# Kernel optimization log

Hardware: AMD Instinct MI355X
Metric: run time of the kernel (lower is better)

The kernel has to match this reference:

```python
import jax, jax.numpy as jnp
import numpy as np

HEAD_DIM = 6
WS = 8  # window size
GROUPS = 4
EPS = 1e-5


def conv3x3(x, w, b):
    y = jax.lax.conv_general_dilated(x, w, (1, 1), [(1, 1), (1, 1)],
                                     dimension_numbers=('NCHW', 'OIHW', 'NCHW'))
    return y + b[None, :, None, None]


def conv1x1(x, w, b):
    # w: (O, C, 1, 1) pointwise conv == channel matmul
    return jnp.einsum('bchw,oc->bohw', x, w[:, :, 0, 0]) + b[None, :, None, None]


def group_norm(x, gamma, beta):
    B, C, H, W = x.shape
    xg = x.reshape(B, GROUPS, C // GROUPS, H, W)
    mu = xg.mean(axis=(2, 3, 4), keepdims=True)
    var = xg.var(axis=(2, 3, 4), keepdims=True)
    xg = (xg - mu) * jax.lax.rsqrt(var + EPS)
    return xg.reshape(B, C, H, W) * gamma[None, :, None, None] + beta[None, :, None, None]


def window_attention(x, qkv_w, qkv_b, proj_w, proj_b):
    # Per-window channel attention (attn is head_dim x head_dim, softmax over last dim).
    B, C, H, W = x.shape
    heads = C // HEAD_DIM
    scale = HEAD_DIM ** -0.5
    Hn, Wn = H // WS, W // WS
    L = WS * WS
    qkv = conv1x1(x, qkv_w, qkv_b)                       # (B, 3C, H, W); 1x1 conv commutes with windowing
    qkv = qkv.reshape(B, 3, heads, HEAD_DIM, Hn, WS, Wn, WS)
    qkv = qkv.transpose(1, 0, 4, 6, 2, 3, 5, 7).reshape(3, B, Hn, Wn, heads, HEAD_DIM, L)
    q, k, v = qkv[0], qkv[1], qkv[2]
    attn = jnp.einsum('bijhdl,bijhel->bijhde', q, k) * scale  # (B,Hn,Wn,heads,hd,hd)
    attn = jax.nn.softmax(attn, axis=-1)
    out = jnp.einsum('bijhde,bijhel->bijhdl', attn, v)
    out = out.reshape(B, Hn, Wn, heads, HEAD_DIM, WS, WS)
    out = out.transpose(0, 3, 4, 1, 5, 2, 6).reshape(B, C, H, W)
    return conv1x1(out, proj_w, proj_b)


def shifted_window_attention(x, qkv_w, qkv_b, proj_w, proj_b):
    B, C, H, W = x.shape
    pad_h = (WS - H % WS) % WS
    pad_w = (WS - W % WS) % WS
    if pad_h or pad_w:
        x = jnp.pad(x, ((0, 0), (0, 0), (0, pad_h), (0, pad_w)), mode='reflect')
    s = WS // 2
    x_sh = jnp.roll(x, shift=(-s, -s), axis=(2, 3))
    x1 = window_attention(x, qkv_w, qkv_b, proj_w, proj_b)
    x2 = window_attention(x_sh, qkv_w, qkv_b, proj_w, proj_b)
    x2 = jnp.roll(x2, shift=(s, s), axis=(2, 3))
    x = (x1 + x2) * 0.5
    return x[:, :, :H, :W]


def setup_inputs() -> dict:
    key = jax.random.key(0)
    ks = jax.random.split(key, 12)
    B, Cin, Cout, T, H, W = 16, 96, 96, 256, 128, 128
    std = 0.05
    return {
        'x': jax.random.normal(ks[0], (B, Cin, H, W), jnp.float32),
        't_emb': jax.random.normal(ks[1], (B, T), jnp.float32),
        'w1': jax.random.normal(ks[2], (Cout, Cin, 3, 3), jnp.float32) * std,
        'b1': jnp.zeros((Cout,), jnp.float32),
        'g1': jnp.ones((Cout,), jnp.float32),
        'be1': jnp.zeros((Cout,), jnp.float32),
        'wt': jax.random.normal(ks[3], (2 * Cout, T), jnp.float32) * std,
        'bt': jnp.zeros((2 * Cout,), jnp.float32),
        'qkv_w': jax.random.normal(ks[4], (3 * Cout, Cout, 1, 1), jnp.float32) * std,
        'qkv_b': jnp.zeros((3 * Cout,), jnp.float32),
        'proj_w': jax.random.normal(ks[5], (Cout, Cout, 1, 1), jnp.float32) * std,
        'proj_b': jnp.zeros((Cout,), jnp.float32),
        'ga': jnp.ones((Cout,), jnp.float32),
        'ba': jnp.zeros((Cout,), jnp.float32),
        'w2': jax.random.normal(ks[6], (Cout, Cout, 3, 3), jnp.float32) * std,
        'b2': jnp.zeros((Cout,), jnp.float32),
        'g2': jnp.ones((Cout,), jnp.float32),
        'be2': jnp.zeros((Cout,), jnp.float32),
    }


def reference(x, t_emb, w1, b1, g1, be1, wt, bt, qkv_w, qkv_b, proj_w, proj_b,
              ga, ba, w2, b2, g2, be2):
    C = w1.shape[0]
    # layer1: conv3x3 -> GN(4) -> SiLU
    h = jax.nn.silu(group_norm(conv3x3(x, w1, b1), g1, be1))
    # time FiLM
    t = jax.nn.silu(t_emb @ wt.T + bt)             # (B, 2C)
    shift, bias = t[:, :C], t[:, C:]
    h = h * (1.0 + shift[:, :, None, None]) + bias[:, :, None, None]
    residual = h
    h = group_norm(h, ga, ba)
    h = shifted_window_attention(h, qkv_w, qkv_b, proj_w, proj_b)
    h = residual + h
    # layer2: conv3x3 -> GN(4) -> SiLU
    h = jax.nn.silu(group_norm(conv3x3(h, w2, b2), g2, be2))
    return h
```

## Files before the change

### kernel.cpp

```cpp
#include <hip/hip_runtime.h>

#define B_   16
#define C_   96
#define H_   128
#define W_   128
#define HW_  16384
#define CPG_ 24
#define NPG_ 393216.0f
#define TDIM_ 256
#define PLANE_ ((size_t)B_ * C_ * HW_)

typedef unsigned short ushort_t;
typedef __bf16 bf16x8 __attribute__((ext_vector_type(8)));
typedef float  f32x4  __attribute__((ext_vector_type(4)));
typedef unsigned short u16x8 __attribute__((ext_vector_type(8)));
typedef unsigned short u16x4 __attribute__((ext_vector_type(4)));

#define ICP 104

__device__ __forceinline__ float silu_f(float x) { return x / (1.f + __expf(-x)); }
__device__ __forceinline__ float bf2f(ushort_t u) {
    union { float f; unsigned int i; } x; x.i = ((unsigned int)u) << 16; return x.f;
}
__device__ __forceinline__ ushort_t f2bf(float f) {
    __bf16 h = (__bf16)f; return *(ushort_t*)&h;
}

__global__ void temb_kernel(const float* __restrict__ t_emb,
                            const float* __restrict__ wt,
                            const float* __restrict__ bt,
                            float* __restrict__ tvec) {
    int idx = blockIdx.x * 256 + threadIdx.x;
    if (idx >= B_ * 192) return;
    int b = idx / 192, o = idx - b * 192;
    float a = bt[o];
    const float* te = t_emb + b * TDIM_;
    const float* wr = wt + o * TDIM_;
    for (int k = 0; k < TDIM_; ++k) a += te[k] * wr[k];
    tvec[idx] = silu_f(a);
}

__global__ void castw_kernel(const float* __restrict__ w1,
                             const float* __restrict__ w2,
                             ushort_t* __restrict__ wbf1,
                             ushort_t* __restrict__ wbf2) {
    int i = blockIdx.x * 256 + threadIdx.x;
    int ic = i % 96;
    int t  = i / 96;
    int oc = t % 96;
    int kk = t / 96;
    int src = (oc * 96 + ic) * 9 + kk;
    wbf1[i] = f2bf(w1[src]);
    wbf2[i] = f2bf(w2[src]);
}

template<int FP32>
__device__ __forceinline__ void stage_row(const void* __restrict__ xin,
                                          ushort_t* __restrict__ ti2,
                                          int b, int gy, int x0, int slot, int tid) {
    const bool rowok = (gy >= 0 && gy < H_);
#pragma unroll
    for (int it = 0; it < 3; ++it) {
        int idx = it * 256 + tid;
        int ic = idx % 96;
        int xc = idx / 96;
        u16x8 v = {};
        if (rowok) {
            if (FP32) {
                const float* xf = (const float*)xin;
                const float4* p = (const float4*)&xf[((size_t)(b * 96 + ic) * H_ + gy) * W_ + x0 + xc * 8];
                float4 f0 = p[0], f1 = p[1];
                v[0] = f2bf(f0.x); v[1] = f2bf(f0.y); v[2] = f2bf(f0.z); v[3] = f2bf(f0.w);
                v[4] = f2bf(f1.x); v[5] = f2bf(f1.y); v[6] = f2bf(f1.z); v[7] = f2bf(f1.w);
            } else {
                const ushort_t* xb = (const ushort_t*)xin;
                v = *(const u16x8*)&xb[((size_t)(b * 96 + ic) * H_ + gy) * W_ + x0 + xc * 8];
            }
        }
        ushort_t* dst = &ti2[(slot * 66 + xc * 8 + 1) * ICP + ic];
#pragma unroll
        for (int j = 0; j < 8; ++j) dst[j * ICP] = v[j];
    }
    if (tid < 192) {
        int ic = tid % 96;
        int side = tid / 96;
        int xi = side ? 65 : 0;
        int gx = x0 - 1 + xi;
        ushort_t vv = 0;
        if (rowok && gx >= 0 && gx < W_) {
            if (FP32) vv = f2bf(((const float*)xin)[((size_t)(b * 96 + ic) * H_ + gy) * W_ + gx]);
            else      vv = ((const ushort_t*)xin)[((size_t)(b * 96 + ic) * H_ + gy) * W_ + gx];
        }
        ti2[(slot * 66 + xi) * ICP + ic] = vv;
    }
}

template<int FP32>
__global__ __launch_bounds__(256, 3)
void conv3x3_mfma_kernel(const void* __restrict__ xin,
                         const ushort_t* __restrict__ wbf,
                         const float* __restrict__ bias,
                         float* __restrict__ out,
                         float* __restrict__ stats) {
    __shared__ __align__(16) ushort_t ti2[2 * 66 * ICP];
    __shared__ __align__(16) ushort_t wc[96 * ICP];
    __shared__ float red[4][96][2];

    const int b   = blockIdx.z;
    const int y0  = blockIdx.y * 2;
    const int x0  = blockIdx.x * 64;
    const int tid = threadIdx.x;
    const int wv   = tid >> 6;
    const int lane = tid & 63;
    const int l15  = lane & 15;
    const int quad = lane >> 4;

    stage_row<FP32>(xin, ti2, b, y0 - 1, x0, 0, tid);
    stage_row<FP32>(xin, ti2, b, y0 + 0, x0, 1, tid);

    int wsrc[5], wdst[5];
#pragma unroll
    for (int i = 0; i < 5; ++i) {
        int idx = tid + i * 256;
        int icb = idx % 12;
        int oc  = idx / 12;
        wsrc[i] = oc * 96 + icb * 8;
        wdst[i] = oc * ICP + icb * 8;
    }
    u16x8 wreg[5];
#pragma unroll
    for (int i = 0; i < 4; ++i) wreg[i] = *(const u16x8*)&wbf[wsrc[i]];
    if (tid < 128) wreg[4] = *(const u16x8*)&wbf[wsrc[4]];

    f32x4 acc[2][6];
#pragma unroll
    for (int m = 0; m < 2; ++m)
#pragma unroll
        for (int nt = 0; nt < 6; ++nt)
            acc[m][nt] = (f32x4){0.f, 0.f, 0.f, 0.f};

#pragma unroll 1
    for (int kk = 0; kk < 9; ++kk) {
        const int ky = (kk >= 6) ? 2 : (kk >= 3 ? 1 : 0);
        const int kx = kk - 3 * ky;
        const int sA = ky & 1;
        const int sB = sA ^ 1;

        __syncthreads();
#pragma unroll
        for (int i = 0; i < 4; ++i) *(u16x8*)&wc[wdst[i]] = wreg[i];
        if (tid < 128) *(u16x8*)&wc[wdst[4]] = wreg[4];
        if (kk == 3)      stage_row<FP32>(xin, ti2, b, y0 + 1, x0, 0, tid);
        else if (kk == 6) stage_row<FP32>(xin, ti2, b, y0 + 2, x0, 1, tid);
        __syncthreads();
        if (kk < 8) {
            const ushort_t* wsk = wbf + (kk + 1) * 9216;
#pragma unroll
            for (int i = 0; i < 4; ++i) wreg[i] = *(const u16x8*)&wsk[wsrc[i]];
            if (tid < 128) wreg[4] = *(const u16x8*)&wsk[wsrc[4]];
        }
#pragma unroll 1
        for (int ck = 0; ck < 3; ++ck) {
            const int kbase = ck * 32 + quad * 8;
            bf16x8 a0 = *(const bf16x8*)&ti2[(sA * 66 + (wv * 16 + l15 + kx)) * ICP + kbase];
            bf16x8 a1 = *(const bf16x8*)&ti2[(sB * 66 + (wv * 16 + l15 + kx)) * ICP + kbase];
#pragma unroll
            for (int nt = 0; nt < 6; ++nt) {
                bf16x8 bv = *(const bf16x8*)&wc[(nt * 16 + l15) * ICP + kbase];
                acc[0][nt] = __builtin_amdgcn_mfma_f32_16x16x32_bf16(a0, bv, acc[0][nt], 0, 0, 0);
                acc[1][nt] = __builtin_amdgcn_mfma_f32_16x16x32_bf16(a1, bv, acc[1][nt], 0, 0, 0);
            }
        }
    }

    float lsum[6], lsq[6];
#pragma unroll
    for (int nt = 0; nt < 6; ++nt) { lsum[nt] = 0.f; lsq[nt] = 0.f; }

#pragma unroll
    for (int m = 0; m < 2; ++m) {
        const int gy = y0 + m;
        const int gx = x0 + wv * 16 + quad * 4;
#pragma unroll
        for (int nt = 0; nt < 6; ++nt) {
            const int oc = nt * 16 + l15;
            const float bz = bias[oc];
            float v0 = acc[m][nt][0] + bz;
            float v1 = acc[m][nt][1] + bz;
            float v2 = acc[m][nt][2] + bz;
            float v3 = acc[m][nt][3] + bz;
            float4 vv = make_float4(v0, v1, v2, v3);
            *(float4*)&out[((size_t)(b * 96 + oc) * H_ + gy) * W_ + gx] = vv;
            lsum[nt] += v0 + v1 + v2 + v3;
            lsq[nt]  += v0 * v0 + v1 * v1 + v2 * v2 + v3 * v3;
        }
    }
#pragma unroll
    for (int nt = 0; nt < 6; ++nt) {
        float s = lsum[nt], q = lsq[nt];
        s += __shfl_down(s, 32, 64);
        s += __shfl_down(s, 16, 64);
        q += __shfl_down(q, 32, 64);
        q += __shfl_down(q, 16, 64);
        if (lane < 16) {
            red[wv][nt * 16 + lane][0] = s;
            red[wv][nt * 16 + lane][1] = q;
        }
    }
    __syncthreads();
    if (tid < 8) {
        const int g = tid >> 1, which = tid & 1;
        float v = 0.f;
        for (int oc = g * CPG_; oc < g * CPG_ + CPG_; ++oc)
            for (int w2 = 0; w2 < 4; ++w2) v += red[w2][oc][which];
        atomicAdd(&stats[(b * 4 + g) * 2 + which], v);
    }
}

__global__ void apply1_kernel(const float* y,
                              const float* __restrict__ stats1,
                              const float* __restrict__ g1,
                              const float* __restrict__ be1,
                              const float* __restrict__ tvec,
                              float* h,
                              float* __restrict__ stats2) {
    const int bc = blockIdx.x;
    const int b = bc / C_, c = bc - b * C_;
    const int g = c / CPG_;
    const float sum = stats1[(b * 4 + g) * 2], sumsq = stats1[(b * 4 + g) * 2 + 1];
    const float mean = sum / NPG_;
    const float var  = sumsq / NPG_ - mean * mean;
    const float rstd = rsqrtf(var + 1e-5f);
    const float sc = rstd * g1[c];
    const float sh = be1[c] - mean * sc;
    const float tsc = 1.f + tvec[b * 192 + c];
    const float tbi = tvec[b * 192 + 96 + c];

    const float4* yp = (const float4*)(y + (size_t)bc * HW_);
    float4* hp = (float4*)(h + (size_t)bc * HW_);
    float ls = 0.f, lss = 0.f;
    for (int i = threadIdx.x; i < HW_ / 4; i += 256) {
        float4 v = yp[i];
        float r0 = silu_f(v.x * sc + sh) * tsc + tbi;
        float r1 = silu_f(v.y * sc + sh) * tsc + tbi;
        float r2 = silu_f(v.z * sc + sh) * tsc + tbi;
        float r3 = silu_f(v.w * sc + sh) * tsc + tbi;
        hp[i] = make_float4(r0, r1, r2, r3);
        ls  += r0 + r1 + r2 + r3;
        lss += r0*r0 + r1*r1 + r2*r2 + r3*r3;
    }
    for (int off = 32; off > 0; off >>= 1) {
        ls  += __shfl_down(ls, off, 64);
        lss += __shfl_down(lss, off, 64);
    }
    if ((threadIdx.x & 63) == 0) {
        atomicAdd(&stats2[(b * 4 + g) * 2 + 0], ls);
        atomicAdd(&stats2[(b * 4 + g) * 2 + 1], lss);
    }
}

__global__ void gn_bf16_kernel(const float* __restrict__ in,
                               const float* __restrict__ stats,
                               const float* __restrict__ gamma,
                               const float* __restrict__ beta,
                               ushort_t* __restrict__ outb) {
    const int bc = blockIdx.x;
    const int b = bc / C_, c = bc - b * C_;
    const int g = c / CPG_;
    const float sum = stats[(b * 4 + g) * 2], sumsq = stats[(b * 4 + g) * 2 + 1];
    const float mean = sum / NPG_;
    const float var  = sumsq / NPG_ - mean * mean;
    const float rstd = rsqrtf(var + 1e-5f);
    const float sc = rstd * gamma[c];
    const float sh = beta[c] - mean * sc;
    const float4* ip = (const float4*)(in + (size_t)bc * HW_);
    ushort4* op = (ushort4*)(outb + (size_t)bc * HW_);
    for (int i = threadIdx.x; i < HW_ / 4; i += 256) {
        float4 v = ip[i];
        ushort4 u = { f2bf(v.x * sc + sh), f2bf(v.y * sc + sh),
                      f2bf(v.z * sc + sh), f2bf(v.w * sc + sh) };
        op[i] = u;
    }
}

__global__ void gn_apply_kernel(const float* in,
                                const float* __restrict__ stats,
                                const float* __restrict__ gamma,
                                const float* __restrict__ beta,
                                float* out, int dosilu) {
    const int bc = blockIdx.x;
    const int b = bc / C_, c = bc - b * C_;
    const int g = c / CPG_;
    const float sum = stats[(b * 4 + g) * 2], sumsq = stats[(b * 4 + g) * 2 + 1];
    const float mean = sum / NPG_;
    const float var  = sumsq / NPG_ - mean * mean;
    const float rstd = rsqrtf(var + 1e-5f);
    const float sc = rstd * gamma[c];
    const float sh = beta[c] - mean * sc;
    const float4* ip = (const float4*)(in + (size_t)bc * HW_);
    float4* op = (float4*)(out + (size_t)bc * HW_);
    for (int i = threadIdx.x; i < HW_ / 4; i += 256) {
        float4 v = ip[i];
        float r0 = v.x * sc + sh, r1 = v.y * sc + sh;
        float r2 = v.z * sc + sh, r3 = v.w * sc + sh;
        if (dosilu) { r0 = silu_f(r0); r1 = silu_f(r1); r2 = silu_f(r2); r3 = silu_f(r3); }
        op[i] = make_float4(r0, r1, r2, r3);
    }
}

__global__ __launch_bounds__(256, 3)
void qkv_gemm_kernel(const ushort_t* __restrict__ xq,
                     const float* __restrict__ qw,
                     const float* __restrict__ qb,
                     ushort_t* __restrict__ qkvbuf) {
    __shared__ __align__(16) ushort_t ti[2 * 64 * ICP];
    __shared__ __align__(16) ushort_t wc[96 * ICP];

    const int bz = blockIdx.z;
    const int b = bz / 3, s = bz - b * 3;
    const int y0 = blockIdx.y * 2;
    const int x0 = blockIdx.x * 64;
    const int tid = threadIdx.x;
    const int wv = tid >> 6, lane = tid & 63;
    const int l15 = lane & 15, quad = lane >> 4;

#pragma unroll
    for (int it = 0; it < 6; ++it) {
        int idx = it * 256 + tid;
        int ic = idx % 96;
        int t2 = idx / 96;
        int xc = t2 & 7;
        int r  = t2 >> 3;
        u16x8 v = *(const u16x8*)&xq[((size_t)(b * 96 + ic) * H_ + y0 + r) * W_ + x0 + xc * 8];
        ushort_t* dst = &ti[(r * 64 + xc * 8) * ICP + ic];
#pragma unroll
        for (int j = 0; j < 8; ++j) dst[j * ICP] = v[j];
    }
#pragma unroll
    for (int it = 0; it < 9; ++it) {
        int idx = it * 256 + tid;
        int icq = idx % 24;
        int oc  = idx / 24;
        float4 wv4 = *(const float4*)&qw[(s * 96 + oc) * 96 + icq * 4];
        ushort4 u = { f2bf(wv4.x), f2bf(wv4.y), f2bf(wv4.z), f2bf(wv4.w) };
        *(ushort4*)&wc[oc * ICP + icq * 4] = u;
    }
    __syncthreads();

    f32x4 acc[2][6];
#pragma unroll
    for (int m = 0; m < 2; ++m)
#pragma unroll
        for (int nt = 0; nt < 6; ++nt) acc[m][nt] = (f32x4){0.f, 0.f, 0.f, 0.f};

#pragma unroll
    for (int ck = 0; ck < 3; ++ck) {
        const int kbase = ck * 32 + quad * 8;
        bf16x8 a0 = *(const bf16x8*)&ti[(0 * 64 + wv * 16 + l15) * ICP + kbase];
        bf16x8 a1 = *(const bf16x8*)&ti[(1 * 64 + wv * 16 + l15) * ICP + kbase];
#pragma unroll
        for (int nt = 0; nt < 6; ++nt) {
            bf16x8 bv = *(const bf16x8*)&wc[(nt * 16 + l15) * ICP + kbase];
            acc[0][nt] = __builtin_amdgcn_mfma_f32_16x16x32_bf16(a0, bv, acc[0][nt], 0, 0, 0);
            acc[1][nt] = __builtin_amdgcn_mfma_f32_16x16x32_bf16(a1, bv, acc[1][nt], 0, 0, 0);
        }
    }

#pragma unroll
    for (int m = 0; m < 2; ++m) {
        const int gy = y0 + m;
        const int gx = x0 + wv * 16 + quad * 4;
#pragma unroll
        for (int nt = 0; nt < 6; ++nt) {
            const int ocg = s * 96 + nt * 16 + l15;
            const float bz2 = qb[ocg];
            ushort4 u = { f2bf(acc[m][nt][0] + bz2), f2bf(acc[m][nt][1] + bz2),
                          f2bf(acc[m][nt][2] + bz2), f2bf(acc[m][nt][3] + bz2) };
            *(ushort4*)&qkvbuf[((size_t)(b * 288 + ocg) * H_ + gy) * W_ + gx] = u;
        }
    }
}

#define QKC 1288
#define QKR 160
#define OSTS 1032
#define VTS 520
__global__ __launch_bounds__(256, 2)
void attn2_kernel(const ushort_t* __restrict__ qkv,
                  ushort_t* __restrict__ obuf, int shift, int accumulate) {
    __shared__ __align__(16) ushort_t qk[12 * QKC];
    __shared__ __align__(16) ushort_t vt[16 * VTS + 32];
    __shared__ __align__(16) ushort_t ost[6 * OSTS];

    const int h = blockIdx.x, wy = blockIdx.y, b = blockIdx.z;
    const int tid = threadIdx.x;
    const int wv = tid >> 6, lane = tid & 63;
    const int l15 = lane & 15, quad = lane >> 4;

    for (int idx = tid; idx < 2304; idx += 256) {
        int xc = idx & 15;
        int t2 = idx >> 4;
        int r  = t2 & 7;
        int ch = t2 >> 3;
        int part = ch / 6, d = ch - part * 6;
        int gch = part * 96 + h * 6 + d;
        int gy = (wy * 8 + r + shift) & 127;
        size_t rowb = ((size_t)(b * 288 + gch) * H_ + gy) * W_;
        ushort4 u0, u1;
        if (shift == 0) {
            u0 = *(const ushort4*)&qkv[rowb + xc * 8];
            u1 = *(const ushort4*)&qkv[rowb + xc * 8 + 4];
        } else {
            u0 = *(const ushort4*)&qkv[rowb + ((xc * 8 + 4) & 127)];
            u1 = *(const ushort4*)&qkv[rowb + ((xc * 8 + 8) & 127)];
        }
        ushort_t* dst = (part < 2) ? &qk[ch * QKC + r * QKR + xc * 8]
                                   : &ost[d * OSTS + r * 128 + xc * 8];
        *(ushort4*)dst = u0;
        *(ushort4*)(dst + 4) = u1;
    }
    __syncthreads();

    {
        const int r   = tid >> 5;
        const int pxq = tid & 31;
        const int px  = pxq * 4;
        u16x4 vv[6];
#pragma unroll
        for (int c = 0; c < 6; ++c)
            vv[c] = *(const u16x4*)&ost[c * OSTS + r * 128 + px];
        const int wx = px >> 3;
        const int p7 = px & 7;
#pragma unroll
        for (int j = 0; j < 4; ++j) {
            u16x8 t;
            t[0] = vv[0][j]; t[1] = vv[1][j]; t[2] = vv[2][j];
            t[3] = vv[3][j]; t[4] = vv[4][j]; t[5] = vv[5][j];
            t[6] = 0; t[7] = 0;
            *(u16x8*)&vt[wx * VTS + (r * 8 + p7 + j) * 8] = t;
        }
        if (tid < 16) ((unsigned int*)(vt + 16 * VTS))[tid] = 0u;
    }
    __syncthreads();

    const float scale = 0.40824829046386302f;
    const int dcl = (l15 < 6) ? l15 : 5;
    const int chA = 6 + dcl;
    const int chB = dcl;

    for (int i = 0; i < 4; ++i) {
        const int wx = wv * 4 + i;
        f32x4 sa = (f32x4){0.f, 0.f, 0.f, 0.f};
#pragma unroll
        for (int ck = 0; ck < 2; ++ck) {
            const int r = ck * 4 + quad;
            bf16x8 af  = *(const bf16x8*)&qk[chA * QKC + r * QKR + wx * 8];
            bf16x8 bfv = *(const bf16x8*)&qk[chB * QKC + r * QKR + wx * 8];
            sa = __builtin_amdgcn_mfma_f32_16x16x32_bf16(af, bfv, sa, 0, 0, 0);
        }
        float s0 = sa[0] * scale, s1 = sa[1] * scale, s2 = sa[2] * scale, s3 = sa[3] * scale;
        float m = -3.4e38f;
        if (quad == 0) m = fmaxf(fmaxf(s0, s1), fmaxf(s2, s3));
        else if (quad == 1) m = fmaxf(s0, s1);
        m = fmaxf(m, __shfl_xor(m, 16, 64));
        m = fmaxf(m, __shfl_xor(m, 32, 64));
        float p0 = (quad <= 1) ? __expf(s0 - m) : 0.f;
        float p1 = (quad <= 1) ? __expf(s1 - m) : 0.f;
        float p2 = (quad == 0) ? __expf(s2 - m) : 0.f;
        float p3 = (quad == 0) ? __expf(s3 - m) : 0.f;
        float sum = p0 + p1 + p2 + p3;
        sum += __shfl_xor(sum, 16, 64);
        sum += __shfl_xor(sum, 32, 64);
        float inv = 1.f / sum;
        p0 *= inv; p1 *= inv; p2 *= inv; p3 *= inv;
        float e4 = __shfl_xor(p0, 16, 64);
        float e5 = __shfl_xor(p1, 16, 64);
        bf16x8 pf;
        pf[0] = (__bf16)p0; pf[1] = (__bf16)p1; pf[2] = (__bf16)p2; pf[3] = (__bf16)p3;
        pf[4] = (__bf16)e4; pf[5] = (__bf16)e5;
        pf[6] = (__bf16)0.f; pf[7] = (__bf16)0.f;
        if (quad != 0) { bf16x8 z = {}; pf = z; }
#pragma unroll
        for (int mt = 0; mt < 4; ++mt) {
            bf16x8 av = *(const bf16x8*)&vt[wx * VTS + (mt * 16 + l15) * 8 + quad * 8];
            f32x4 o = __builtin_amdgcn_mfma_f32_16x16x32_bf16(av, pf, (f32x4){0.f,0.f,0.f,0.f}, 0, 0, 0);
            if (l15 < 6) {
                const int px = mt * 16 + quad * 4;
                const int r = px >> 3, c = px & 7;
                ushort4 st = { f2bf(o[0]), f2bf(o[1]), f2bf(o[2]), f2bf(o[3]) };
                *(ushort4*)&ost[l15 * OSTS + r * 128 + wx * 8 + c] = st;
            }
        }
    }
    __syncthreads();

    for (int idx = tid; idx < 768; idx += 256) {
        int xc = idx & 15;
        int t2 = idx >> 4;
        int r = t2 & 7, d = t2 >> 3;
        int gy = (wy * 8 + r + shift) & 127;
        size_t rowb = ((size_t)(b * 96 + h * 6 + d) * H_ + gy) * W_;
        size_t a0, a1;
        if (shift == 0) { a0 = rowb + xc * 8; a1 = rowb + xc * 8 + 4; }
        else { a0 = rowb + ((xc * 8 + 4) & 127); a1 = rowb + ((xc * 8 + 8) & 127); }
        const ushort_t* src = &ost[d * OSTS + r * 128 + xc * 8];
        ushort4 v0 = *(const ushort4*)src;
        ushort4 v1 = *(const ushort4*)(src + 4);
        if (accumulate) {
            ushort4 q0 = *(const ushort4*)&obuf[a0];
            ushort4 q1 = *(const ushort4*)&obuf[a1];
            v0.x = f2bf(0.5f * (bf2f(v0.x) + bf2f(q0.x)));
            v0.y = f2bf(0.5f * (bf2f(v0.y) + bf2f(q0.y)));
            v0.z = f2bf(0.5f * (bf2f(v0.z) + bf2f(q0.z)));
            v0.w = f2bf(0.5f * (bf2f(v0.w) + bf2f(q0.w)));
            v1.x = f2bf(0.5f * (bf2f(v1.x) + bf2f(q1.x)));
            v1.y = f2bf(0.5f * (bf2f(v1.y) + bf2f(q1.y)));
            v1.z = f2bf(0.5f * (bf2f(v1.z) + bf2f(q1.z)));
            v1.w = f2bf(0.5f * (bf2f(v1.w) + bf2f(q1.w)));
        }
        *(ushort4*)&obuf[a0] = v0;
        *(ushort4*)&obuf[a1] = v1;
    }
}

__global__ __launch_bounds__(256, 3)
void proj_gemm_kernel(const ushort_t* __restrict__ ob,
                      const float* __restrict__ pw,
                      const float* __restrict__ pb,
                      const float* __restrict__ resid,
                      ushort_t* __restrict__ h2) {
    __shared__ __align__(16) ushort_t ti[2 * 64 * ICP];
    __shared__ __align__(16) ushort_t wc[96 * ICP];

    const int b = blockIdx.z;
    const int y0 = blockIdx.y * 2;
    const int x0 = blockIdx.x * 64;
    const int tid = threadIdx.x;
    const int wv = tid >> 6, lane = tid & 63;
    const int l15 = lane & 15, quad = lane >> 4;

#pragma unroll
    for (int it = 0; it < 6; ++it) {
        int idx = it * 256 + tid;
        int ic = idx % 96;
        int t2 = idx / 96;
        int xc = t2 & 7;
        int r  = t2 >> 3;
        u16x8 v = *(const u16x8*)&ob[((size_t)(b * 96 + ic) * H_ + y0 + r) * W_ + x0 + xc * 8];
        ushort_t* dst = &ti[(r * 64 + xc * 8) * ICP + ic];
#pragma unroll
        for (int j = 0; j < 8; ++j) dst[j * ICP] = v[j];
    }
#pragma unroll
    for (int it = 0; it < 9; ++it) {
        int idx = it * 256 + tid;
        int icq = idx % 24;
        int oc  = idx / 24;
        float4 wv4 = *(const float4*)&pw[oc * 96 + icq * 4];
        ushort4 u = { f2bf(wv4.x), f2bf(wv4.y), f2bf(wv4.z), f2bf(wv4.w) };
        *(ushort4*)&wc[oc * ICP + icq * 4] = u;
    }
    __syncthreads();

    f32x4 acc[2][6];
#pragma unroll
    for (int m = 0; m < 2; ++m)
#pragma unroll
        for (int nt = 0; nt < 6; ++nt) acc[m][nt] = (f32x4){0.f, 0.f, 0.f, 0.f};

#pragma unroll
    for (int ck = 0; ck < 3; ++ck) {
        const int kbase = ck * 32 + quad * 8;
        bf16x8 a0 = *(const bf16x8*)&ti[(0 * 64 + wv * 16 + l15) * ICP + kbase];
        bf16x8 a1 = *(const bf16x8*)&ti[(1 * 64 + wv * 16 + l15) * ICP + kbase];
#pragma unroll
        for (int nt = 0; nt < 6; ++nt) {
            bf16x8 bv = *(const bf16x8*)&wc[(nt * 16 + l15) * ICP + kbase];
            acc[0][nt] = __builtin_amdgcn_mfma_f32_16x16x32_bf16(a0, bv, acc[0][nt], 0, 0, 0);
            acc[1][nt] = __builtin_amdgcn_mfma_f32_16x16x32_bf16(a1, bv, acc[1][nt], 0, 0, 0);
        }
    }

#pragma unroll
    for (int m = 0; m < 2; ++m) {
        const int gy = y0 + m;
        const int gx = x0 + wv * 16 + quad * 4;
#pragma unroll
        for (int nt = 0; nt < 6; ++nt) {
            const int oc = nt * 16 + l15;
            const float bz2 = pb[oc];
            size_t addr = ((size_t)(b * 96 + oc) * H_ + gy) * W_ + gx;
            float4 rv = *(const float4*)&resid[addr];
            ushort4 u = { f2bf(acc[m][nt][0] + bz2 + rv.x),
                          f2bf(acc[m][nt][1] + bz2 + rv.y),
                          f2bf(acc[m][nt][2] + bz2 + rv.z),
                          f2bf(acc[m][nt][3] + bz2 + rv.w) };
            *(ushort4*)&h2[addr] = u;
        }
    }
}

extern "C" void kernel_launch(void* const* d_in, const int* in_sizes, int n_in,
                              void* d_out, int out_size, void* d_ws, size_t ws_size,
                              hipStream_t stream) {
    const float* x     = (const float*)d_in[0];
    const float* t_emb = (const float*)d_in[1];
    const float* w1    = (const float*)d_in[2];
    const float* b1    = (const float*)d_in[3];
    const float* g1    = (const float*)d_in[4];
    const float* be1   = (const float*)d_in[5];
    const float* wt    = (const float*)d_in[6];
    const float* bt    = (const float*)d_in[7];
    const float* qkv_w = (const float*)d_in[8];
    const float* qkv_b = (const float*)d_in[9];
    const float* proj_w= (const float*)d_in[10];
    const float* proj_b= (const float*)d_in[11];
    const float* ga    = (const float*)d_in[12];
    const float* ba    = (const float*)d_in[13];
    const float* w2    = (const float*)d_in[14];
    const float* b2    = (const float*)d_in[15];
    const float* g2    = (const float*)d_in[16];
    const float* be2   = (const float*)d_in[17];

    float* out = (float*)d_out;

    ushort_t* A  = (ushort_t*)d_ws;
    ushort_t* Bq = A + PLANE_;
    float* stats = (float*)(Bq + 3 * PLANE_);
    float* tvec  = stats + 384;
    ushort_t* wbf1 = (ushort_t*)(tvec + 3072);
    ushort_t* wbf2 = wbf1 + 82944;

    hipMemsetAsync(stats, 0, 384 * sizeof(float), stream);
    temb_kernel<<<12, 256, 0, stream>>>(t_emb, wt, bt, tvec);
    castw_kernel<<<324, 256, 0, stream>>>(w1, w2, wbf1, wbf2);

    conv3x3_mfma_kernel<1><<<dim3(2, 64, 16), 256, 0, stream>>>((const void*)x, wbf1, b1, out, stats);

    apply1_kernel<<<B_ * C_, 256, 0, stream>>>(out, stats, g1, be1, tvec, out, stats + 128);
    gn_bf16_kernel<<<B_ * C_, 256, 0, stream>>>(out, stats + 128, ga, ba, A);

    qkv_gemm_kernel<<<dim3(2, 64, 48), 256, 0, stream>>>(A, qkv_w, qkv_b, Bq);

    attn2_kernel<<<dim3(16, 16, 16), 256, 0, stream>>>(Bq, A, 0, 0);
    attn2_kernel<<<dim3(16, 16, 16), 256, 0, stream>>>(Bq, A, 4, 1);

    proj_gemm_kernel<<<dim3(2, 64, 16), 256, 0, stream>>>(A, proj_w, proj_b, out, Bq);

    conv3x3_mfma_kernel<0><<<dim3(2, 64, 16), 256, 0, stream>>>((const void*)Bq, wbf2, b2, out, stats + 256);

    gn_apply_kernel<<<B_ * C_, 256, 0, stream>>>(out, stats + 256, g2, be2, out, 1);
}
```

Before: 727.1 us.

## Load conv3x3 weights straight into registers in MFMA layout with 4-row tiles

Weights are now pre-permuted on the host-side cast kernel into the per-lane MFMA fragment order, so each lane reads its B fragments directly from global memory into registers with double-buffered prefetch. This removes the shared-memory weight staging and the two barriers per filter tap. Each block now computes four output rows instead of two, using a 4-slot rolling row buffer, which halves the grid and reuses each weight fragment across more MFMAs. The cost is more accumulator registers (occupancy hint lowered to 2 blocks) and weight reads that go to global or L2 per block rather than shared memory.

```diff
diff --git a/kernel.cpp b/kernel.cpp
--- a/kernel.cpp
+++ b/kernel.cpp
@@ -45,10 +45,14 @@
                              ushort_t* __restrict__ wbf1,
                              ushort_t* __restrict__ wbf2) {
     int i = blockIdx.x * 256 + threadIdx.x;
-    int ic = i % 96;
-    int t  = i / 96;
-    int oc = t % 96;
-    int kk = t / 96;
+    int j    = i & 7;
+    int lane = (i >> 3) & 63;
+    int t    = i >> 9;
+    int nt   = t % 6;
+    int ks   = t / 6;
+    int kk   = ks / 3, ck = ks - 3 * kk;
+    int oc = nt * 16 + (lane & 15);
+    int ic = ck * 32 + (lane >> 4) * 8 + j;
     int src = (oc * 96 + ic) * 9 + kk;
     wbf1[i] = f2bf(w1[src]);
     wbf2[i] = f2bf(w2[src]);
@@ -96,18 +100,17 @@
 }
 
 template<int FP32>
-__global__ __launch_bounds__(256, 3)
+__global__ __launch_bounds__(256, 2)
 void conv3x3_mfma_kernel(const void* __restrict__ xin,
                          const ushort_t* __restrict__ wbf,
                          const float* __restrict__ bias,
                          float* __restrict__ out,
                          float* __restrict__ stats) {
-    __shared__ __align__(16) ushort_t ti2[2 * 66 * ICP];
-    __shared__ __align__(16) ushort_t wc[96 * ICP];
+    __shared__ __align__(16) ushort_t ti2[4 * 66 * ICP];
     __shared__ float red[4][96][2];
 
     const int b   = blockIdx.z;
-    const int y0  = blockIdx.y * 2;
+    const int y0  = blockIdx.y * 4;
     const int x0  = blockIdx.x * 64;
     const int tid = threadIdx.x;
     const int wv   = tid >> 6;
@@ -117,60 +120,61 @@
 
     stage_row<FP32>(xin, ti2, b, y0 - 1, x0, 0, tid);
     stage_row<FP32>(xin, ti2, b, y0 + 0, x0, 1, tid);
-
-    int wsrc[5], wdst[5];
-#pragma unroll
-    for (int i = 0; i < 5; ++i) {
-        int idx = tid + i * 256;
-        int icb = idx % 12;
-        int oc  = idx / 12;
-        wsrc[i] = oc * 96 + icb * 8;
-        wdst[i] = oc * ICP + icb * 8;
-    }
-    u16x8 wreg[5];
-#pragma unroll
-    for (int i = 0; i < 4; ++i) wreg[i] = *(const u16x8*)&wbf[wsrc[i]];
-    if (tid < 128) wreg[4] = *(const u16x8*)&wbf[wsrc[4]];
-
-    f32x4 acc[2][6];
-#pragma unroll
-    for (int m = 0; m < 2; ++m)
+    stage_row<FP32>(xin, ti2, b, y0 + 1, x0, 2, tid);
+    stage_row<FP32>(xin, ti2, b, y0 + 2, x0, 3, tid);
+
+    const ushort_t* wrp = wbf + (size_t)lane * 8;
+
+    bf16x8 wA[6], wB[6];
+#pragma unroll
+    for (int nt = 0; nt < 6; ++nt)
+        wA[nt] = *(const bf16x8*)&wrp[nt * 512];
+
+    f32x4 acc[4][6];
+#pragma unroll
+    for (int m = 0; m < 4; ++m)
 #pragma unroll
         for (int nt = 0; nt < 6; ++nt)
             acc[m][nt] = (f32x4){0.f, 0.f, 0.f, 0.f};
 
-#pragma unroll 1
-    for (int kk = 0; kk < 9; ++kk) {
-        const int ky = (kk >= 6) ? 2 : (kk >= 3 ? 1 : 0);
-        const int kx = kk - 3 * ky;
-        const int sA = ky & 1;
-        const int sB = sA ^ 1;
-
-        __syncthreads();
-#pragma unroll
-        for (int i = 0; i < 4; ++i) *(u16x8*)&wc[wdst[i]] = wreg[i];
-        if (tid < 128) *(u16x8*)&wc[wdst[4]] = wreg[4];
-        if (kk == 3)      stage_row<FP32>(xin, ti2, b, y0 + 1, x0, 0, tid);
-        else if (kk == 6) stage_row<FP32>(xin, ti2, b, y0 + 2, x0, 1, tid);
-        __syncthreads();
-        if (kk < 8) {
-            const ushort_t* wsk = wbf + (kk + 1) * 9216;
-#pragma unroll
-            for (int i = 0; i < 4; ++i) wreg[i] = *(const u16x8*)&wsk[wsrc[i]];
-            if (tid < 128) wreg[4] = *(const u16x8*)&wsk[wsrc[4]];
-        }
-#pragma unroll 1
-        for (int ck = 0; ck < 3; ++ck) {
-            const int kbase = ck * 32 + quad * 8;
-            bf16x8 a0 = *(const bf16x8*)&ti2[(sA * 66 + (wv * 16 + l15 + kx)) * ICP + kbase];
-            bf16x8 a1 = *(const bf16x8*)&ti2[(sB * 66 + (wv * 16 + l15 + kx)) * ICP + kbase];
-#pragma unroll
-            for (int nt = 0; nt < 6; ++nt) {
-                bf16x8 bv = *(const bf16x8*)&wc[(nt * 16 + l15) * ICP + kbase];
-                acc[0][nt] = __builtin_amdgcn_mfma_f32_16x16x32_bf16(a0, bv, acc[0][nt], 0, 0, 0);
-                acc[1][nt] = __builtin_amdgcn_mfma_f32_16x16x32_bf16(a1, bv, acc[1][nt], 0, 0, 0);
-            }
-        }
+    __syncthreads();
+
+    auto body = [&](int ks, bf16x8 (&cur)[6], bf16x8 (&nxt)[6]) {
+        const int kk = ks / 3, ck = ks - 3 * kk;
+        const int ky = kk / 3, kx = kk - 3 * ky;
+        if (ks < 26) {
+#pragma unroll
+            for (int nt = 0; nt < 6; ++nt)
+                nxt[nt] = *(const bf16x8*)&wrp[((ks + 1) * 6 + nt) * 512];
+        }
+        const int kbase = ck * 32 + quad * 8;
+        bf16x8 a[4];
+#pragma unroll
+        for (int m = 0; m < 4; ++m) {
+            const int slot = (m + ky) & 3;
+            a[m] = *(const bf16x8*)&ti2[(slot * 66 + wv * 16 + l15 + kx) * ICP + kbase];
+        }
+#pragma unroll
+        for (int nt = 0; nt < 6; ++nt)
+#pragma unroll
+            for (int m = 0; m < 4; ++m)
+                acc[m][nt] = __builtin_amdgcn_mfma_f32_16x16x32_bf16(a[m], cur[nt], acc[m][nt], 0, 0, 0);
+    };
+
+#pragma unroll
+    for (int ks = 0; ks < 27; ++ks) {
+        if (ks == 9) {
+            __syncthreads();
+            stage_row<FP32>(xin, ti2, b, y0 + 3, x0, 0, tid);
+            __syncthreads();
+        }
+        if (ks == 18) {
+            __syncthreads();
+            stage_row<FP32>(xin, ti2, b, y0 + 4, x0, 1, tid);
+            __syncthreads();
+        }
+        if (ks & 1) body(ks, wB, wA);
+        else        body(ks, wA, wB);
     }
 
     float lsum[6], lsq[6];
@@ -178,7 +182,7 @@
     for (int nt = 0; nt < 6; ++nt) { lsum[nt] = 0.f; lsq[nt] = 0.f; }
 
 #pragma unroll
-    for (int m = 0; m < 2; ++m) {
+    for (int m = 0; m < 4; ++m) {
         const int gy = y0 + m;
         const int gx = x0 + wv * 16 + quad * 4;
 #pragma unroll
@@ -635,7 +639,7 @@
     temb_kernel<<<12, 256, 0, stream>>>(t_emb, wt, bt, tvec);
     castw_kernel<<<324, 256, 0, stream>>>(w1, w2, wbf1, wbf2);
 
-    conv3x3_mfma_kernel<1><<<dim3(2, 64, 16), 256, 0, stream>>>((const void*)x, wbf1, b1, out, stats);
+    conv3x3_mfma_kernel<1><<<dim3(2, 32, 16), 256, 0, stream>>>((const void*)x, wbf1, b1, out, stats);
 
     apply1_kernel<<<B_ * C_, 256, 0, stream>>>(out, stats, g1, be1, tvec, out, stats + 128);
     gn_bf16_kernel<<<B_ * C_, 256, 0, stream>>>(out, stats + 128, ga, ba, A);
@@ -647,7 +651,7 @@
 
     proj_gemm_kernel<<<dim3(2, 64, 16), 256, 0, stream>>>(A, proj_w, proj_b, out, Bq);
 
-    conv3x3_mfma_kernel<0><<<dim3(2, 64, 16), 256, 0, stream>>>((const void*)Bq, wbf2, b2, out, stats + 256);
+    conv3x3_mfma_kernel<0><<<dim3(2, 32, 16), 256, 0, stream>>>((const void*)Bq, wbf2, b2, out, stats + 256);
 
     gn_apply_kernel<<<B_ * C_, 256, 0, stream>>>(out, stats + 256, g2, be2, out, 1);
 }
```

New measurement: 738.3 us. No clear change (+1.5%).
